# Performance work log

Hardware: AMD Instinct MI355X
Metric: run time of the kernel (lower is better)

## Reference

```python
import jax, jax.numpy as jnp
import numpy as np

EPS = 1e-5
ROPE_BASE = 10000.0


def _layernorm(x, g, b):
    mu = jnp.mean(x, axis=-1, keepdims=True)
    var = jnp.mean(jnp.square(x - mu), axis=-1, keepdims=True)
    return (x - mu) * jax.lax.rsqrt(var + EPS) * g + b


def _rope(q, k):
    # q, k: (B, T, H, D); rotate interleaved pairs along last dim, positions over T
    T, D = q.shape[1], q.shape[-1]
    half = D // 2
    inv_freq = ROPE_BASE ** (-jnp.arange(half, dtype=jnp.float32) / half)
    ang = jnp.arange(T, dtype=jnp.float32)[:, None] * inv_freq  # (T, half)
    cos = jnp.cos(ang)[None, :, None, :]
    sin = jnp.sin(ang)[None, :, None, :]

    def rot(x):
        xr, xi = x[..., 0::2], x[..., 1::2]
        yr = xr * cos - xi * sin
        yi = xr * sin + xi * cos
        return jnp.stack([yr, yi], axis=-1).reshape(x.shape)

    return rot(q), rot(k)


def setup_inputs() -> dict:
    key = jax.random.key(0)
    ks = jax.random.split(key, 5)
    E, F, B, T = 1024, 4096, 2, 2048
    s = 0.02
    return {
        "x": jax.random.normal(ks[0], (B, T, E), jnp.float32),
        "in_proj_w": jax.random.normal(ks[1], (3 * E, E), jnp.float32) * s,
        "out_proj_w": jax.random.normal(ks[2], (E, E), jnp.float32) * s,
        "ln1_g": jnp.ones((E,), jnp.float32),
        "ln1_b": jnp.zeros((E,), jnp.float32),
        "ln2_g": jnp.ones((E,), jnp.float32),
        "ln2_b": jnp.zeros((E,), jnp.float32),
        "w1": jax.random.normal(ks[3], (F, E), jnp.float32) * s,
        "w2": jax.random.normal(ks[4], (E, F), jnp.float32) * s,
        "context": 256,
    }


def reference(x, in_proj_w, out_proj_w, ln1_g, ln1_b, ln2_g, ln2_b, w1, w2, context):
    B, T, E = x.shape
    H = 16
    D = E // H

    # ---- self-attention block (pre-norm, residual) ----
    h = _layernorm(x, ln1_g, ln1_b)
    proj = h @ in_proj_w.T  # (B, T, 3E)
    qkv = proj.reshape(B, T, 3, H, D)
    q = qkv[:, :, 0]  # (B, T, H, D)
    k = qkv[:, :, 1]
    v = qkv[:, :, 2].transpose(0, 2, 1, 3)  # (B, H, T, D)
    q, k = _rope(q, k)
    q = q.transpose(0, 2, 1, 3)  # (B, H, T, D)
    k = k.transpose(0, 2, 1, 3)

    pos = jnp.arange(T)
    delta = pos[:, None] - pos[None, :]  # (T, T)
    mask = (delta >= 0) & (delta < context)

    scores = jnp.einsum("bhtd,bhsd->bhts", q, k) / jnp.sqrt(jnp.float32(D))
    scores = jnp.where(mask[None, None], scores, jnp.float32(-1e30))
    attn = jax.nn.softmax(scores, axis=-1)
    o = jnp.einsum("bhts,bhsd->bhtd", attn, v)
    o = o.transpose(0, 2, 1, 3).reshape(B, T, E)
    x = x + o @ out_proj_w.T

    # ---- FFN block (pre-norm, residual) ----
    h = _layernorm(x, ln2_g, ln2_b)
    update = jax.nn.gelu(h @ w1.T, approximate=False) @ w2.T
    return x + update
```

## Files before the change

### kernel.cpp

```cpp
#include <hip/hip_runtime.h>
#include <math.h>

#define B_BATCH 2
#define T_SEQ   2048
#define E_DIM   1024
#define H_HEADS 16
#define D_HEAD  64
#define F_DIM   4096
#define M_ROWS  (B_BATCH * T_SEQ)

typedef __attribute__((ext_vector_type(8))) short short8;
typedef __attribute__((ext_vector_type(4))) float floatx4;
typedef __attribute__((ext_vector_type(8))) unsigned short ushortx8;

typedef __attribute__((address_space(1))) const void global_cvoid;
typedef __attribute__((address_space(3))) void lds_void;

__device__ __forceinline__ unsigned short f2bf(float f) {
    unsigned u = __float_as_uint(f);
    u += 0x7fffu + ((u >> 16) & 1u);
    return (unsigned short)(u >> 16);
}
__device__ __forceinline__ float bf2f(unsigned short h) {
    return __uint_as_float(((unsigned)h) << 16);
}

__device__ __forceinline__ unsigned lds_lo(const void* p) {
    return (unsigned)(unsigned long long)p;
}

__device__ __forceinline__ float gelu_f(float v) {
    const float x = fabsf(v) * 0.70710678118654752f;
    const float t = __builtin_amdgcn_rcpf(__builtin_fmaf(0.3275911f, x, 1.0f));
    float p = __builtin_fmaf(1.061405429f, t, -1.453152027f);
    p = __builtin_fmaf(p, t, 1.421413741f);
    p = __builtin_fmaf(p, t, -0.284496736f);
    p = __builtin_fmaf(p, t, 0.254829592f);
    p *= t;
    const float e = __expf(-x * x);
    float er = __builtin_fmaf(-p, e, 1.0f);
    er = copysignf(er, v);
    return 0.5f * v * (1.0f + er);
}

__device__ __forceinline__ float waveReduceSum(float v) {
#pragma unroll
    for (int off = 32; off > 0; off >>= 1) v += __shfl_xor(v, off, 64);
    return v;
}

__global__ __launch_bounds__(256) void cvt_kernel(const float* __restrict__ in,
                                                  unsigned short* __restrict__ out,
                                                  int n) {
    const int i = (blockIdx.x * 256 + threadIdx.x) * 4;
    if (i >= n) return;
    float4 v = *(const float4*)(in + i);
    ushort4 o;
    o.x = f2bf(v.x); o.y = f2bf(v.y); o.z = f2bf(v.z); o.w = f2bf(v.w);
    *(ushort4*)(out + i) = o;
}

__global__ __launch_bounds__(256) void reduce4_kernel(const float* __restrict__ p,
                                                      float* __restrict__ out, int n) {
    const int i = (blockIdx.x * 256 + threadIdx.x) * 4;
    if (i >= n) return;
    float4 a  = *(const float4*)(out + i);
    float4 b0 = *(const float4*)(p + i);
    float4 b1 = *(const float4*)(p + (size_t)n + i);
    float4 b2 = *(const float4*)(p + 2 * (size_t)n + i);
    float4 b3 = *(const float4*)(p + 3 * (size_t)n + i);
    a.x += b0.x + b1.x + b2.x + b3.x;
    a.y += b0.y + b1.y + b2.y + b3.y;
    a.z += b0.z + b1.z + b2.z + b3.z;
    a.w += b0.w + b1.w + b2.w + b3.w;
    *(float4*)(out + i) = a;
}

__global__ __launch_bounds__(256) void rope_tab_kernel(float* __restrict__ tab) {
    const int idx = blockIdx.x * 256 + threadIdx.x;
    const int pos = idx >> 5, i = idx & 31;
    const float invf = powf(10000.0f, -(float)i / 32.0f);
    const float ang = (float)pos * invf;
    tab[idx * 2]     = cosf(ang);
    tab[idx * 2 + 1] = sinf(ang);
}

__global__ __launch_bounds__(256) void ln_kernel(const float* __restrict__ x,
                                                 const float* __restrict__ g,
                                                 const float* __restrict__ b,
                                                 unsigned short* __restrict__ out) {
    const int row = blockIdx.x;
    const float* xr = x + (size_t)row * E_DIM;
    float4 v = ((const float4*)xr)[threadIdx.x];
    float s  = v.x + v.y + v.z + v.w;
    float sq = v.x * v.x + v.y * v.y + v.z * v.z + v.w * v.w;

    __shared__ float red[8];
    float ws_ = waveReduceSum(s);
    float wq  = waveReduceSum(sq);
    int wid = threadIdx.x >> 6;
    if ((threadIdx.x & 63) == 0) { red[wid] = ws_; red[wid + 4] = wq; }
    __syncthreads();
    float ts = red[0] + red[1] + red[2] + red[3];
    float tq = red[4] + red[5] + red[6] + red[7];
    float mean = ts * (1.0f / E_DIM);
    float var  = tq * (1.0f / E_DIM) - mean * mean;
    float inv  = rsqrtf(var + 1e-5f);

    float4 gv = ((const float4*)g)[threadIdx.x];
    float4 bv = ((const float4*)b)[threadIdx.x];
    ushort4 o;
    o.x = f2bf((v.x - mean) * inv * gv.x + bv.x);
    o.y = f2bf((v.y - mean) * inv * gv.y + bv.y);
    o.z = f2bf((v.z - mean) * inv * gv.z + bv.z);
    o.w = f2bf((v.w - mean) * inv * gv.w + bv.w);
    ((ushort4*)(out + (size_t)row * E_DIM))[threadIdx.x] = o;
}

template <int EPI>
__global__ __launch_bounds__(256) void gemm_bf16(const unsigned short* __restrict__ A,
                                                 const unsigned short* __restrict__ Wt,
                                                 const float* __restrict__ R,
                                                 float* __restrict__ Cf,
                                                 unsigned short* __restrict__ Cb,
                                                 int M, int N, int K) {
    __shared__ unsigned short As[128 * 64];
    __shared__ unsigned short Bs[128 * 64];
    const int tid  = threadIdx.x;
    const int wave = tid >> 6, lane = tid & 63;
    const int wm   = wave >> 1, wn = wave & 1;
    const int quad = lane >> 4, l16 = lane & 15;
    const int m0 = blockIdx.y * 128, n0 = blockIdx.x * 128;
    const int Kc   = K / gridDim.z;
    const int kbeg = blockIdx.z * Kc;

    const int row_rel = lane >> 3;
    const int ch      = lane & 7;

    const floatx4 z = {0.0f, 0.0f, 0.0f, 0.0f};
    floatx4 acc[4][4];
#pragma unroll
    for (int i = 0; i < 4; ++i)
#pragma unroll
        for (int j = 0; j < 4; ++j) acc[i][j] = z;

    for (int k0 = kbeg; k0 < kbeg + Kc; k0 += 64) {
        __syncthreads();
#pragma unroll
        for (int i = 0; i < 4; ++i) {
            const int chunk = wave * 4 + i;
            const int grow  = chunk * 8 + row_rel;
            const int lch   = ch ^ (grow & 7);
            const unsigned short* ga = A  + (size_t)(m0 + grow) * K + k0 + lch * 8;
            const unsigned short* gb = Wt + (size_t)(n0 + grow) * K + k0 + lch * 8;
            __builtin_amdgcn_global_load_lds((global_cvoid*)ga,
                                             (lds_void*)(As + chunk * 512), 16, 0, 0);
            __builtin_amdgcn_global_load_lds((global_cvoid*)gb,
                                             (lds_void*)(Bs + chunk * 512), 16, 0, 0);
        }
        __syncthreads();

#pragma unroll
        for (int ks = 0; ks < 2; ++ks) {
            short8 af[4], bfr[4];
#pragma unroll
            for (int mt = 0; mt < 4; ++mt) {
                const int r = wm * 64 + mt * 16 + l16;
                const int p = (ks * 4 + quad) ^ (r & 7);
                af[mt] = *(const short8*)(As + r * 64 + p * 8);
            }
#pragma unroll
            for (int nt = 0; nt < 4; ++nt) {
                const int r = wn * 64 + nt * 16 + l16;
                const int p = (ks * 4 + quad) ^ (r & 7);
                bfr[nt] = *(const short8*)(Bs + r * 64 + p * 8);
            }
#pragma unroll
            for (int mt = 0; mt < 4; ++mt)
#pragma unroll
                for (int nt = 0; nt < 4; ++nt)
                    acc[mt][nt] = __builtin_amdgcn_mfma_f32_16x16x32_bf16(
                        af[mt], bfr[nt], acc[mt][nt], 0, 0, 0);
        }
    }

#pragma unroll
    for (int mt = 0; mt < 4; ++mt) {
        const int rb = m0 + wm * 64 + mt * 16 + quad * 4;
#pragma unroll
        for (int nt = 0; nt < 4; ++nt) {
            const int col = n0 + wn * 64 + nt * 16 + l16;
#pragma unroll
            for (int r = 0; r < 4; ++r) {
                const size_t idx = (size_t)(rb + r) * N + col;
                const float v = acc[mt][nt][r];
                if (EPI == 1) {
                    Cf[idx] = v + R[idx];
                } else {
                    Cf[idx] = v;
                }
            }
        }
    }
}

template <int EPI>
__global__ __launch_bounds__(512, 2) void gemm256_bf16(const unsigned short* __restrict__ A,
                                                       const unsigned short* __restrict__ Wt,
                                                       float* __restrict__ Cf,
                                                       unsigned short* __restrict__ Cb,
                                                       int M, int N, int K) {
    __shared__ __align__(16) unsigned short Ls[4 * 16384];

    const int tid  = threadIdx.x;
    const int wave = tid >> 6, lane = tid & 63;
    const int wm   = wave >> 2, wn = wave & 3;
    const int quad = lane >> 4, l16 = lane & 15;

    int bid = blockIdx.y * gridDim.x + blockIdx.x;
    const int cpx = (gridDim.x * gridDim.y) >> 3;
    bid = (bid & 7) * cpx + (bid >> 3);
    const int bx = bid % gridDim.x, by = bid / gridDim.x;
    const int m0 = by * 256, n0 = bx * 256;

    const int Kc   = K / gridDim.z;
    const int kbeg = blockIdx.z * Kc;
    const int NT   = Kc >> 5;

    const int rr = lane >> 2;
    const int ch = lane & 3;

    const floatx4 z = {0.0f, 0.0f, 0.0f, 0.0f};
    floatx4 acc[8][4];
#pragma unroll
    for (int i = 0; i < 8; ++i)
#pragma unroll
        for (int j = 0; j < 4; ++j) acc[i][j] = z;

    auto STAGE = [&](int t, int bi) {
        const int k0 = kbeg + t * 32;
#pragma unroll
        for (int i = 0; i < 2; ++i) {
            const int g    = wave * 2 + i;
            const int grow = g * 16 + rr;
            const int sch  = (ch ^ ((grow >> 1) & 3)) * 8;
            const unsigned short* ga = A  + (size_t)(m0 + grow) * K + k0 + sch;
            const unsigned short* gb = Wt + (size_t)(n0 + grow) * K + k0 + sch;
            unsigned short* la = Ls + bi * 16384 + g * 512;
            __builtin_amdgcn_global_load_lds((global_cvoid*)ga, (lds_void*)la,        16, 0, 0);
            __builtin_amdgcn_global_load_lds((global_cvoid*)gb, (lds_void*)(la + 8192), 16, 0, 0);
        }
    };

    const unsigned swz = (unsigned)(quad ^ ((l16 >> 1) & 3));
    const unsigned aA = lds_lo(Ls) + (unsigned)(wm * 128 + l16) * 64u + swz * 16u;
    const unsigned aB = lds_lo(Ls) + 16384u + (unsigned)(wn * 64 + l16) * 64u + swz * 16u;

#define GSTEP(T, C, PD, DOPF, WSTR, DOBAR)                                     \
    do {                                                                       \
        if (DOPF) STAGE((T) + 3, (PD));                                        \
        const unsigned aAc = aA + (C) * 32768u;                                \
        const unsigned aBc = aB + (C) * 32768u;                                \
        short8 af[8], bfr[4];                                                  \
        _Pragma("unroll")                                                      \
        for (int mt = 0; mt < 8; ++mt)                                         \
            asm volatile("ds_read_b128 %0, %1"                                 \
                         : "=v"(af[mt]) : "v"(aAc + mt * 1024u));              \
        _Pragma("unroll")                                                      \
        for (int nt = 0; nt < 4; ++nt)                                         \
            asm volatile("ds_read_b128 %0, %1"                                 \
                         : "=v"(bfr[nt]) : "v"(aBc + nt * 1024u));             \
        asm volatile("s_waitcnt lgkmcnt(0)" ::: "memory");                     \
        __builtin_amdgcn_sched_barrier(0);                                     \
        __builtin_amdgcn_s_setprio(1);                                         \
        _Pragma("unroll")                                                      \
        for (int mt = 0; mt < 8; ++mt)                                         \
            _Pragma("unroll")                                                  \
            for (int nt = 0; nt < 4; ++nt)                                     \
                acc[mt][nt] = __builtin_amdgcn_mfma_f32_16x16x32_bf16(         \
                    af[mt], bfr[nt], acc[mt][nt], 0, 0, 0);                    \
        __builtin_amdgcn_s_setprio(0);                                         \
        if (DOBAR) {                                                           \
            asm volatile("s_waitcnt " WSTR ::: "memory");                      \
            __builtin_amdgcn_s_barrier();                                      \
            __builtin_amdgcn_sched_barrier(0);                                 \
        }                                                                      \
    } while (0)

    STAGE(0, 0);
    STAGE(1, 1);
    STAGE(2, 2);
    asm volatile("s_waitcnt vmcnt(8)" ::: "memory");
    __builtin_amdgcn_s_barrier();
    __builtin_amdgcn_sched_barrier(0);

    int t = 0;
    for (; t + 4 < NT; t += 4) {
        GSTEP(t + 0, 0, 3, true, "vmcnt(8)", true);
        GSTEP(t + 1, 1, 0, true, "vmcnt(8)", true);
        GSTEP(t + 2, 2, 1, true, "vmcnt(8)", true);
        GSTEP(t + 3, 3, 2, true, "vmcnt(8)", true);
    }
    GSTEP(t + 0, 0, 3, true,  "vmcnt(8)", true);
    GSTEP(t + 1, 1, 0, false, "vmcnt(4)", true);
    GSTEP(t + 2, 2, 1, false, "vmcnt(0)", true);
    GSTEP(t + 3, 3, 2, false, "vmcnt(0)", false);
#undef GSTEP

    const size_t zoff = (size_t)blockIdx.z * M * N;
#pragma unroll
    for (int mt = 0; mt < 8; ++mt) {
        const int rb = m0 + wm * 128 + mt * 16 + quad * 4;
#pragma unroll
        for (int nt = 0; nt < 4; ++nt) {
            const int col = n0 + wn * 64 + nt * 16 + l16;
#pragma unroll
            for (int r = 0; r < 4; ++r) {
                const size_t idx = (size_t)(rb + r) * N + col;
                const float v = acc[mt][nt][r];
                if (EPI == 2) {
                    Cb[idx] = f2bf(gelu_f(v));
                } else if (EPI == 4) {
                    Cb[idx] = f2bf(v);
                } else {
                    Cf[zoff + idx] = v;
                }
            }
        }
    }
}

__global__ __launch_bounds__(256) void vtrans_kernel(const unsigned short* __restrict__ proj,
                                                     unsigned short* __restrict__ vt) {
    __shared__ unsigned short L[64 * 72];
    const int bh = blockIdx.y, b = bh >> 4, h = bh & 15;
    const int st = blockIdx.x * 64;
    const int tid = threadIdx.x;
    {
        const int srel = tid >> 2, d16 = (tid & 3) * 16;
        const unsigned short* src =
            proj + (size_t)(b * T_SEQ + st + srel) * (3 * E_DIM) + 2 * E_DIM + h * 64 + d16;
        *(short8*)(L + srel * 72 + d16)     = *(const short8*)(src);
        *(short8*)(L + srel * 72 + d16 + 8) = *(const short8*)(src + 8);
    }
    __syncthreads();
    {
        const int d = tid >> 2, s16 = (tid & 3) * 16;
        short8 o0, o1;
#pragma unroll
        for (int j = 0; j < 8; ++j) {
            o0[j] = (short)L[(s16 + j) * 72 + d];
            o1[j] = (short)L[(s16 + 8 + j) * 72 + d];
        }
        unsigned short* dst = vt + (size_t)(bh * 64 + d) * T_SEQ + st + s16;
        *(short8*)dst       = o0;
        *(short8*)(dst + 8) = o1;
    }
}

__device__ __forceinline__ void rope16(ushortx8 x0, ushortx8 x1, const float* tp,
                                       short8& y0, short8& y1) {
#pragma unroll
    for (int j = 0; j < 4; ++j) {
        const float c = tp[2 * j], s = tp[2 * j + 1];
        const float xr = bf2f(x0[2 * j]), xi = bf2f(x0[2 * j + 1]);
        y0[2 * j]     = (short)f2bf(xr * c - xi * s);
        y0[2 * j + 1] = (short)f2bf(xr * s + xi * c);
    }
#pragma unroll
    for (int j = 0; j < 4; ++j) {
        const float c = tp[8 + 2 * j], s = tp[8 + 2 * j + 1];
        const float xr = bf2f(x1[2 * j]), xi = bf2f(x1[2 * j + 1]);
        y1[2 * j]     = (short)f2bf(xr * c - xi * s);
        y1[2 * j + 1] = (short)f2bf(xr * s + xi * c);
    }
}

__global__ __launch_bounds__(256) void attn_kernel(const unsigned short* __restrict__ proj,
                                                   const unsigned short* __restrict__ vt,
                                                   const float* __restrict__ tab,
                                                   const int* __restrict__ ctxp,
                                                   unsigned short* __restrict__ o) {
    __shared__ unsigned short Qs[64 * 64];
    __shared__ unsigned short Ks[64 * 64];
    __shared__ unsigned short Vs[64 * 64];
    __shared__ unsigned short Ps[4][16 * 64];

    const int ctx = ctxp[0];
    const int tid = threadIdx.x;
    const int wave = tid >> 6, lane = tid & 63;
    const int quad = lane >> 4, l16 = lane & 15;
    const int bh = blockIdx.y, b = bh >> 4, h = bh & 15;
    const int t0 = blockIdx.x * 64;

    {
        const int r = tid >> 2, d16 = (tid & 3) * 16;
        const int pos = t0 + r;
        const unsigned short* src =
            proj + (size_t)(b * T_SEQ + pos) * (3 * E_DIM) + h * 64 + d16;
        ushortx8 x0 = *(const ushortx8*)src;
        ushortx8 x1 = *(const ushortx8*)(src + 8);
        const float* tp = tab + ((size_t)pos * 32 + (d16 >> 1)) * 2;
        short8 y0, y1;
        rope16(x0, x1, tp, y0, y1);
        const int c0 = (tid & 3) * 2;
        *(short8*)(Qs + r * 64 + ((c0)     ^ (r & 7)) * 8) = y0;
        *(short8*)(Qs + r * 64 + ((c0 + 1) ^ (r & 7)) * 8) = y1;
    }

    int first = t0 - (ctx - 1);
    if (first < 0) first = 0;
    const int first_base = first & ~63;

    float m[4] = {-1e30f, -1e30f, -1e30f, -1e30f};
    float l[4] = {0.0f, 0.0f, 0.0f, 0.0f};
    const floatx4 z = {0.0f, 0.0f, 0.0f, 0.0f};
    floatx4 accO[4] = {z, z, z, z};

    const int q_row0 = t0 + wave * 16 + quad * 4;

    for (int s_base = first_base; s_base <= t0; s_base += 64) {
        __syncthreads();
        {
            const int r = tid >> 2, d16 = (tid & 3) * 16;
            const int pos = s_base + r;
            const unsigned short* src =
                proj + (size_t)(b * T_SEQ + pos) * (3 * E_DIM) + E_DIM + h * 64 + d16;
            ushortx8 x0 = *(const ushortx8*)src;
            ushortx8 x1 = *(const ushortx8*)(src + 8);
            const float* tp = tab + ((size_t)pos * 32 + (d16 >> 1)) * 2;
            short8 y0, y1;
            rope16(x0, x1, tp, y0, y1);
            const int c0 = (tid & 3) * 2;
            *(short8*)(Ks + r * 64 + ((c0)     ^ (r & 7)) * 8) = y0;
            *(short8*)(Ks + r * 64 + ((c0 + 1) ^ (r & 7)) * 8) = y1;
        }
#pragma unroll
        for (int i = 0; i < 2; ++i) {
            const int chunk = (wave * 2 + i) * 64 + lane;
            const int d = chunk >> 3, c = chunk & 7;
            const unsigned short* gsrc =
                vt + (size_t)(bh * 64 + d) * T_SEQ + s_base + ((c ^ (d & 7)) * 8);
            __builtin_amdgcn_global_load_lds((global_cvoid*)gsrc,
                                             (lds_void*)(Vs + (wave * 2 + i) * 512),
                                             16, 0, 0);
        }
        __syncthreads();

        floatx4 accS[4] = {z, z, z, z};
#pragma unroll
        for (int ks = 0; ks < 2; ++ks) {
            const int qrow = wave * 16 + l16;
            short8 aq = *(const short8*)(Qs + qrow * 64 + (((ks * 4 + quad) ^ (qrow & 7)) * 8));
#pragma unroll
            for (int nt = 0; nt < 4; ++nt) {
                const int kro = nt * 16 + l16;
                short8 bk = *(const short8*)(Ks + kro * 64 + (((ks * 4 + quad) ^ (kro & 7)) * 8));
                accS[nt] = __builtin_amdgcn_mfma_f32_16x16x32_bf16(aq, bk, accS[nt], 0, 0, 0);
            }
        }

        float p[4][4];
        float alpha[4];
#pragma unroll
        for (int r = 0; r < 4; ++r) {
            const int qa = q_row0 + r;
            float sv[4];
            float vmax = -1e30f;
#pragma unroll
            for (int nt = 0; nt < 4; ++nt) {
                const int sa = s_base + nt * 16 + l16;
                const int dd = qa - sa;
                const bool ok = (unsigned)dd < (unsigned)ctx;
                const float s = ok ? accS[nt][r] * 0.125f : -1e30f;
                sv[nt] = s;
                vmax = fmaxf(vmax, s);
            }
            vmax = fmaxf(vmax, __shfl_xor(vmax, 1));
            vmax = fmaxf(vmax, __shfl_xor(vmax, 2));
            vmax = fmaxf(vmax, __shfl_xor(vmax, 4));
            vmax = fmaxf(vmax, __shfl_xor(vmax, 8));
            const float mn = fmaxf(m[r], vmax);
            alpha[r] = __expf(m[r] - mn);
            float ps = 0.0f;
#pragma unroll
            for (int nt = 0; nt < 4; ++nt) {
                const float pe = (sv[nt] > -0.5e30f) ? __expf(sv[nt] - mn) : 0.0f;
                p[nt][r] = pe;
                ps += pe;
            }
            ps += __shfl_xor(ps, 1);
            ps += __shfl_xor(ps, 2);
            ps += __shfl_xor(ps, 4);
            ps += __shfl_xor(ps, 8);
            l[r] = l[r] * alpha[r] + ps;
            m[r] = mn;
        }

#pragma unroll
        for (int nt = 0; nt < 4; ++nt) {
#pragma unroll
            for (int r = 0; r < 4; ++r) {
                const int row = quad * 4 + r;
                const int col = nt * 16 + l16;
                Ps[wave][row * 64 + (((col >> 3) ^ (row & 7)) * 8) + (col & 7)] =
                    f2bf(p[nt][r]);
            }
        }
#pragma unroll
        for (int nt = 0; nt < 4; ++nt)
#pragma unroll
            for (int r = 0; r < 4; ++r) accO[nt][r] *= alpha[r];

#pragma unroll
        for (int ks = 0; ks < 2; ++ks) {
            short8 ap = *(const short8*)(&Ps[wave][l16 * 64 + (((ks * 4 + quad) ^ (l16 & 7)) * 8)]);
#pragma unroll
            for (int nt = 0; nt < 4; ++nt) {
                const int dr = nt * 16 + l16;
                short8 bv = *(const short8*)(Vs + dr * 64 + (((ks * 4 + quad) ^ (dr & 7)) * 8));
                accO[nt] = __builtin_amdgcn_mfma_f32_16x16x32_bf16(ap, bv, accO[nt], 0, 0, 0);
            }
        }
    }

    float inv[4];
#pragma unroll
    for (int r = 0; r < 4; ++r) inv[r] = 1.0f / l[r];
#pragma unroll
    for (int nt = 0; nt < 4; ++nt) {
#pragma unroll
        for (int r = 0; r < 4; ++r) {
            const int t = q_row0 + r;
            o[(size_t)(b * T_SEQ + t) * E_DIM + h * 64 + nt * 16 + l16] =
                f2bf(accO[nt][r] * inv[r]);
        }
    }
}

extern "C" void kernel_launch(void* const* d_in, const int* in_sizes, int n_in,
                              void* d_out, int out_size, void* d_ws, size_t ws_size,
                              hipStream_t stream) {
    const float* x          = (const float*)d_in[0];
    const float* in_proj_w  = (const float*)d_in[1];
    const float* out_proj_w = (const float*)d_in[2];
    const float* ln1_g      = (const float*)d_in[3];
    const float* ln1_b      = (const float*)d_in[4];
    const float* ln2_g      = (const float*)d_in[5];
    const float* ln2_b      = (const float*)d_in[6];
    const float* w1         = (const float*)d_in[7];
    const float* w2         = (const float*)d_in[8];
    const int*   ctx        = (const int*)d_in[9];
    float* out = (float*)d_out;
    float* ws  = (float*)d_ws;

    const size_t MEG = 1024u * 1024u;
    unsigned short* u = (unsigned short*)ws;
    unsigned short* wqkv_b = u;
    unsigned short* wout_b = u + 3 * MEG;
    unsigned short* w1_b   = u + 4 * MEG;
    unsigned short* h_b    = u + 8 * MEG;
    unsigned short* obuf_b = u + 12 * MEG;
    unsigned short* proj_b = u + 16 * MEG;
    unsigned short* vt_b   = u + 28 * MEG;
    unsigned short* mid_b  = u + 32 * MEG;
    unsigned short* w2_b   = u + 48 * MEG;
    float* tab  = ws + 26 * MEG;
    float* part = ws;

    cvt_kernel<<<3 * E_DIM * E_DIM / 1024, 256, 0, stream>>>(in_proj_w, wqkv_b, 3 * E_DIM * E_DIM);
    cvt_kernel<<<E_DIM * E_DIM / 1024, 256, 0, stream>>>(out_proj_w, wout_b, E_DIM * E_DIM);
    cvt_kernel<<<F_DIM * E_DIM / 1024, 256, 0, stream>>>(w1, w1_b, F_DIM * E_DIM);
    cvt_kernel<<<E_DIM * F_DIM / 1024, 256, 0, stream>>>(w2, w2_b, E_DIM * F_DIM);
    rope_tab_kernel<<<T_SEQ * 32 / 256, 256, 0, stream>>>(tab);

    ln_kernel<<<M_ROWS, 256, 0, stream>>>(x, ln1_g, ln1_b, h_b);
    gemm256_bf16<4><<<dim3(3 * E_DIM / 256, M_ROWS / 256), 512, 0, stream>>>(
        h_b, wqkv_b, nullptr, proj_b, M_ROWS, 3 * E_DIM, E_DIM);
    vtrans_kernel<<<dim3(T_SEQ / 64, B_BATCH * H_HEADS), 256, 0, stream>>>(proj_b, vt_b);
    attn_kernel<<<dim3(T_SEQ / 64, B_BATCH * H_HEADS), 256, 0, stream>>>(
        proj_b, vt_b, tab, ctx, obuf_b);
    gemm_bf16<1><<<dim3(E_DIM / 128, M_ROWS / 128), 256, 0, stream>>>(
        obuf_b, wout_b, x, out, nullptr, M_ROWS, E_DIM, E_DIM);
    ln_kernel<<<M_ROWS, 256, 0, stream>>>(out, ln2_g, ln2_b, h_b);
    gemm256_bf16<2><<<dim3(F_DIM / 256, M_ROWS / 256), 512, 0, stream>>>(
        h_b, w1_b, nullptr, mid_b, M_ROWS, F_DIM, E_DIM);
    gemm256_bf16<5><<<dim3(E_DIM / 256, M_ROWS / 256, 4), 512, 0, stream>>>(
        mid_b, w2_b, part, nullptr, M_ROWS, E_DIM, F_DIM);
    reduce4_kernel<<<M_ROWS * E_DIM / 1024, 256, 0, stream>>>(
        part, out, M_ROWS * E_DIM);
}
```

Measured before the change: 325.5 us.

## Fuse prep kernels and restructure 256-tile GEMM to double-buffered BK=64

```diff
diff --git a/kernel.cpp b/kernel.cpp
--- a/kernel.cpp
+++ b/kernel.cpp
@@ -49,15 +49,74 @@
     return v;
 }
 
-__global__ __launch_bounds__(256) void cvt_kernel(const float* __restrict__ in,
-                                                  unsigned short* __restrict__ out,
-                                                  int n) {
-    const int i = (blockIdx.x * 256 + threadIdx.x) * 4;
-    if (i >= n) return;
-    float4 v = *(const float4*)(in + i);
+__device__ __forceinline__ void ln_row(const float* __restrict__ x,
+                                       const float* __restrict__ g,
+                                       const float* __restrict__ b,
+                                       unsigned short* __restrict__ out, int row) {
+    const float* xr = x + (size_t)row * E_DIM;
+    float4 v = ((const float4*)xr)[threadIdx.x];
+    float s  = v.x + v.y + v.z + v.w;
+    float sq = v.x * v.x + v.y * v.y + v.z * v.z + v.w * v.w;
+
+    __shared__ float red[8];
+    float ws_ = waveReduceSum(s);
+    float wq  = waveReduceSum(sq);
+    int wid = threadIdx.x >> 6;
+    if ((threadIdx.x & 63) == 0) { red[wid] = ws_; red[wid + 4] = wq; }
+    __syncthreads();
+    float ts = red[0] + red[1] + red[2] + red[3];
+    float tq = red[4] + red[5] + red[6] + red[7];
+    float mean = ts * (1.0f / E_DIM);
+    float var  = tq * (1.0f / E_DIM) - mean * mean;
+    float inv  = rsqrtf(var + 1e-5f);
+
+    float4 gv = ((const float4*)g)[threadIdx.x];
+    float4 bv = ((const float4*)b)[threadIdx.x];
     ushort4 o;
-    o.x = f2bf(v.x); o.y = f2bf(v.y); o.z = f2bf(v.z); o.w = f2bf(v.w);
-    *(ushort4*)(out + i) = o;
+    o.x = f2bf((v.x - mean) * inv * gv.x + bv.x);
+    o.y = f2bf((v.y - mean) * inv * gv.y + bv.y);
+    o.z = f2bf((v.z - mean) * inv * gv.z + bv.z);
+    o.w = f2bf((v.w - mean) * inv * gv.w + bv.w);
+    ((ushort4*)(out + (size_t)row * E_DIM))[threadIdx.x] = o;
+}
+
+__global__ __launch_bounds__(256) void ln_kernel(const float* __restrict__ x,
+                                                 const float* __restrict__ g,
+                                                 const float* __restrict__ b,
+                                                 unsigned short* __restrict__ out) {
+    ln_row(x, g, b, out, blockIdx.x);
+}
+
+__global__ __launch_bounds__(256) void prep_kernel(
+    const float* __restrict__ in_proj_w, const float* __restrict__ out_proj_w,
+    const float* __restrict__ w1, const float* __restrict__ w2,
+    const float* __restrict__ x, const float* __restrict__ ln1_g,
+    const float* __restrict__ ln1_b,
+    unsigned short* __restrict__ wqkv_b, unsigned short* __restrict__ wout_b,
+    unsigned short* __restrict__ w1_b, unsigned short* __restrict__ w2_b,
+    unsigned short* __restrict__ h_b, float* __restrict__ tab) {
+    const int blk = blockIdx.x;
+    if (blk < 12288) {
+        const float* src; unsigned short* dst; int base;
+        if (blk < 3072)      { src = in_proj_w;  dst = wqkv_b; base = blk; }
+        else if (blk < 4096) { src = out_proj_w; dst = wout_b; base = blk - 3072; }
+        else if (blk < 8192) { src = w1;         dst = w1_b;   base = blk - 4096; }
+        else                 { src = w2;         dst = w2_b;   base = blk - 8192; }
+        const int i = (base * 256 + threadIdx.x) * 4;
+        float4 v = *(const float4*)(src + i);
+        ushort4 o;
+        o.x = f2bf(v.x); o.y = f2bf(v.y); o.z = f2bf(v.z); o.w = f2bf(v.w);
+        *(ushort4*)(dst + i) = o;
+    } else if (blk < 12544) {
+        const int idx = (blk - 12288) * 256 + threadIdx.x;
+        const int pos = idx >> 5, i = idx & 31;
+        const float invf = powf(10000.0f, -(float)i / 32.0f);
+        const float ang = (float)pos * invf;
+        tab[idx * 2]     = cosf(ang);
+        tab[idx * 2 + 1] = sinf(ang);
+    } else {
+        ln_row(x, ln1_g, ln1_b, h_b, blk - 12544);
+    }
 }
 
 __global__ __launch_bounds__(256) void reduce4_kernel(const float* __restrict__ p,
@@ -74,47 +133,6 @@
     a.z += b0.z + b1.z + b2.z + b3.z;
     a.w += b0.w + b1.w + b2.w + b3.w;
     *(float4*)(out + i) = a;
-}
-
-__global__ __launch_bounds__(256) void rope_tab_kernel(float* __restrict__ tab) {
-    const int idx = blockIdx.x * 256 + threadIdx.x;
-    const int pos = idx >> 5, i = idx & 31;
-    const float invf = powf(10000.0f, -(float)i / 32.0f);
-    const float ang = (float)pos * invf;
-    tab[idx * 2]     = cosf(ang);
-    tab[idx * 2 + 1] = sinf(ang);
-}
-
-__global__ __launch_bounds__(256) void ln_kernel(const float* __restrict__ x,
-                                                 const float* __restrict__ g,
-                                                 const float* __restrict__ b,
-                                                 unsigned short* __restrict__ out) {
-    const int row = blockIdx.x;
-    const float* xr = x + (size_t)row * E_DIM;
-    float4 v = ((const float4*)xr)[threadIdx.x];
-    float s  = v.x + v.y + v.z + v.w;
-    float sq = v.x * v.x + v.y * v.y + v.z * v.z + v.w * v.w;
-
-    __shared__ float red[8];
-    float ws_ = waveReduceSum(s);
-    float wq  = waveReduceSum(sq);
-    int wid = threadIdx.x >> 6;
-    if ((threadIdx.x & 63) == 0) { red[wid] = ws_; red[wid + 4] = wq; }
-    __syncthreads();
-    float ts = red[0] + red[1] + red[2] + red[3];
-    float tq = red[4] + red[5] + red[6] + red[7];
-    float mean = ts * (1.0f / E_DIM);
-    float var  = tq * (1.0f / E_DIM) - mean * mean;
-    float inv  = rsqrtf(var + 1e-5f);
-
-    float4 gv = ((const float4*)g)[threadIdx.x];
-    float4 bv = ((const float4*)b)[threadIdx.x];
-    ushort4 o;
-    o.x = f2bf((v.x - mean) * inv * gv.x + bv.x);
-    o.y = f2bf((v.y - mean) * inv * gv.y + bv.y);
-    o.z = f2bf((v.z - mean) * inv * gv.z + bv.z);
-    o.w = f2bf((v.w - mean) * inv * gv.w + bv.w);
-    ((ushort4*)(out + (size_t)row * E_DIM))[threadIdx.x] = o;
 }
 
 template <int EPI>
@@ -210,7 +228,7 @@
                                                        float* __restrict__ Cf,
                                                        unsigned short* __restrict__ Cb,
                                                        int M, int N, int K) {
-    __shared__ __align__(16) unsigned short Ls[4 * 16384];
+    __shared__ __align__(16) unsigned short Ls[2 * 32768];
 
     const int tid  = threadIdx.x;
     const int wave = tid >> 6, lane = tid & 63;
@@ -225,10 +243,10 @@
 
     const int Kc   = K / gridDim.z;
     const int kbeg = blockIdx.z * Kc;
-    const int NT   = Kc >> 5;
-
-    const int rr = lane >> 2;
-    const int ch = lane & 3;
+    const int NT   = Kc >> 6;
+
+    const int rr8 = lane >> 3;
+    const int ch8 = lane & 7;
 
     const floatx4 z = {0.0f, 0.0f, 0.0f, 0.0f};
     floatx4 acc[8][4];
@@ -238,38 +256,64 @@
         for (int j = 0; j < 4; ++j) acc[i][j] = z;
 
     auto STAGE = [&](int t, int bi) {
-        const int k0 = kbeg + t * 32;
-#pragma unroll
-        for (int i = 0; i < 2; ++i) {
-            const int g    = wave * 2 + i;
-            const int grow = g * 16 + rr;
-            const int sch  = (ch ^ ((grow >> 1) & 3)) * 8;
-            const unsigned short* ga = A  + (size_t)(m0 + grow) * K + k0 + sch;
-            const unsigned short* gb = Wt + (size_t)(n0 + grow) * K + k0 + sch;
-            unsigned short* la = Ls + bi * 16384 + g * 512;
-            __builtin_amdgcn_global_load_lds((global_cvoid*)ga, (lds_void*)la,        16, 0, 0);
-            __builtin_amdgcn_global_load_lds((global_cvoid*)gb, (lds_void*)(la + 8192), 16, 0, 0);
+        const int k0 = kbeg + t * 64;
+#pragma unroll
+        for (int i = 0; i < 4; ++i) {
+            const int ca   = wave * 4 + i;
+            const int grow = ca * 8 + rr8;
+            const int lch  = ch8 ^ (grow & 7);
+            const unsigned short* ga = A  + (size_t)(m0 + grow) * K + k0 + lch * 8;
+            const unsigned short* gb = Wt + (size_t)(n0 + grow) * K + k0 + lch * 8;
+            unsigned short* la = Ls + bi * 32768 + ca * 512;
+            __builtin_amdgcn_global_load_lds((global_cvoid*)ga, (lds_void*)la, 16, 0, 0);
+            __builtin_amdgcn_global_load_lds((global_cvoid*)gb,
+                                             (lds_void*)(la + 16384), 16, 0, 0);
         }
     };
 
-    const unsigned swz = (unsigned)(quad ^ ((l16 >> 1) & 3));
-    const unsigned aA = lds_lo(Ls) + (unsigned)(wm * 128 + l16) * 64u + swz * 16u;
-    const unsigned aB = lds_lo(Ls) + 16384u + (unsigned)(wn * 64 + l16) * 64u + swz * 16u;
-
-#define GSTEP(T, C, PD, DOPF, WSTR, DOBAR)                                     \
+    const unsigned e3  = (unsigned)(l16 & 7);
+    const unsigned rA  = (unsigned)(wm * 128 + l16) * 128u;
+    const unsigned rB  = (unsigned)(wn * 64 + l16) * 128u;
+    const unsigned aA0 = lds_lo(Ls) + rA + ((unsigned)quad ^ e3) * 16u;
+    const unsigned aA1 = lds_lo(Ls) + rA + ((unsigned)(4 + quad) ^ e3) * 16u;
+    const unsigned aB0 = lds_lo(Ls) + 32768u + rB + ((unsigned)quad ^ e3) * 16u;
+    const unsigned aB1 = lds_lo(Ls) + 32768u + rB + ((unsigned)(4 + quad) ^ e3) * 16u;
+
+#define GSTEP(T, C, DOPF, DOBAR)                                               \
     do {                                                                       \
-        if (DOPF) STAGE((T) + 3, (PD));                                        \
-        const unsigned aAc = aA + (C) * 32768u;                                \
-        const unsigned aBc = aB + (C) * 32768u;                                \
-        short8 af[8], bfr[4];                                                  \
+        short8 a0[8], b0[4], a1[8], b1[4];                                     \
+        const unsigned uA0 = aA0 + (C) * 65536u;                               \
+        const unsigned uB0 = aB0 + (C) * 65536u;                               \
+        const unsigned uA1 = aA1 + (C) * 65536u;                               \
+        const unsigned uB1 = aB1 + (C) * 65536u;                               \
         _Pragma("unroll")                                                      \
         for (int mt = 0; mt < 8; ++mt)                                         \
             asm volatile("ds_read_b128 %0, %1"                                 \
-                         : "=v"(af[mt]) : "v"(aAc + mt * 1024u));              \
+                         : "=v"(a0[mt]) : "v"(uA0 + mt * 2048u));              \
         _Pragma("unroll")                                                      \
         for (int nt = 0; nt < 4; ++nt)                                         \
             asm volatile("ds_read_b128 %0, %1"                                 \
-                         : "=v"(bfr[nt]) : "v"(aBc + nt * 1024u));             \
+                         : "=v"(b0[nt]) : "v"(uB0 + nt * 2048u));              \
+        if (DOPF) STAGE((T) + 1, (C) ^ 1);                                     \
+        asm volatile("s_waitcnt lgkmcnt(0)" ::: "memory");                     \
+        __builtin_amdgcn_sched_barrier(0);                                     \
+        _Pragma("unroll")                                                      \
+        for (int mt = 0; mt < 8; ++mt)                                         \
+            asm volatile("ds_read_b128 %0, %1"                                 \
+                         : "=v"(a1[mt]) : "v"(uA1 + mt * 2048u));              \
+        _Pragma("unroll")                                                      \
+        for (int nt = 0; nt < 4; ++nt)                                         \
+            asm volatile("ds_read_b128 %0, %1"                                 \
+                         : "=v"(b1[nt]) : "v"(uB1 + nt * 2048u));              \
+        __builtin_amdgcn_sched_barrier(0);                                     \
+        __builtin_amdgcn_s_setprio(1);                                         \
+        _Pragma("unroll")                                                      \
+        for (int mt = 0; mt < 8; ++mt)                                         \
+            _Pragma("unroll")                                                  \
+            for (int nt = 0; nt < 4; ++nt)                                     \
+                acc[mt][nt] = __builtin_amdgcn_mfma_f32_16x16x32_bf16(         \
+                    a0[mt], b0[nt], acc[mt][nt], 0, 0, 0);                     \
+        __builtin_amdgcn_s_setprio(0);                                         \
         asm volatile("s_waitcnt lgkmcnt(0)" ::: "memory");                     \
         __builtin_amdgcn_sched_barrier(0);                                     \
         __builtin_amdgcn_s_setprio(1);                                         \
@@ -278,33 +322,27 @@
             _Pragma("unroll")                                                  \
             for (int nt = 0; nt < 4; ++nt)                                     \
                 acc[mt][nt] = __builtin_amdgcn_mfma_f32_16x16x32_bf16(         \
-                    af[mt], bfr[nt], acc[mt][nt], 0, 0, 0);                    \
+                    a1[mt], b1[nt], acc[mt][nt], 0, 0, 0);                     \
         __builtin_amdgcn_s_setprio(0);                                         \
         if (DOBAR) {                                                           \
-            asm volatile("s_waitcnt " WSTR ::: "memory");                      \
+            asm volatile("s_waitcnt vmcnt(0)" ::: "memory");                   \
             __builtin_amdgcn_s_barrier();                                      \
             __builtin_amdgcn_sched_barrier(0);                                 \
         }                                                                      \
     } while (0)
 
     STAGE(0, 0);
-    STAGE(1, 1);
-    STAGE(2, 2);
-    asm volatile("s_waitcnt vmcnt(8)" ::: "memory");
+    asm volatile("s_waitcnt vmcnt(0)" ::: "memory");
     __builtin_amdgcn_s_barrier();
     __builtin_amdgcn_sched_barrier(0);
 
     int t = 0;
-    for (; t + 4 < NT; t += 4) {
-        GSTEP(t + 0, 0, 3, true, "vmcnt(8)", true);
-        GSTEP(t + 1, 1, 0, true, "vmcnt(8)", true);
-        GSTEP(t + 2, 2, 1, true, "vmcnt(8)", true);
-        GSTEP(t + 3, 3, 2, true, "vmcnt(8)", true);
-    }
-    GSTEP(t + 0, 0, 3, true,  "vmcnt(8)", true);
-    GSTEP(t + 1, 1, 0, false, "vmcnt(4)", true);
-    GSTEP(t + 2, 2, 1, false, "vmcnt(0)", true);
-    GSTEP(t + 3, 3, 2, false, "vmcnt(0)", false);
+    for (; t < NT - 2; t += 2) {
+        GSTEP(t + 0, 0, true, true);
+        GSTEP(t + 1, 1, true, true);
+    }
+    GSTEP(t + 0, 0, true, true);
+    GSTEP(t + 1, 1, false, false);
 #undef GSTEP
 
     const size_t zoff = (size_t)blockIdx.z * M * N;
@@ -568,13 +606,9 @@
     float* tab  = ws + 26 * MEG;
     float* part = ws;
 
-    cvt_kernel<<<3 * E_DIM * E_DIM / 1024, 256, 0, stream>>>(in_proj_w, wqkv_b, 3 * E_DIM * E_DIM);
-    cvt_kernel<<<E_DIM * E_DIM / 1024, 256, 0, stream>>>(out_proj_w, wout_b, E_DIM * E_DIM);
-    cvt_kernel<<<F_DIM * E_DIM / 1024, 256, 0, stream>>>(w1, w1_b, F_DIM * E_DIM);
-    cvt_kernel<<<E_DIM * F_DIM / 1024, 256, 0, stream>>>(w2, w2_b, E_DIM * F_DIM);
-    rope_tab_kernel<<<T_SEQ * 32 / 256, 256, 0, stream>>>(tab);
-
-    ln_kernel<<<M_ROWS, 256, 0, stream>>>(x, ln1_g, ln1_b, h_b);
+    prep_kernel<<<16640, 256, 0, stream>>>(in_proj_w, out_proj_w, w1, w2,
+                                           x, ln1_g, ln1_b,
+                                           wqkv_b, wout_b, w1_b, w2_b, h_b, tab);
     gemm256_bf16<4><<<dim3(3 * E_DIM / 256, M_ROWS / 256), 512, 0, stream>>>(
         h_b, wqkv_b, nullptr, proj_b, M_ROWS, 3 * E_DIM, E_DIM);
     vtrans_kernel<<<dim3(T_SEQ / 64, B_BATCH * H_HEADS), 256, 0, stream>>>(proj_b, vt_b);
```

Result: slower. 484.9 us (+48.9%).
